# Kernel optimization log

Measured on AMD Instinct MI355X. Metric: run time of the kernel, lower is better.

Reference implementation:

```python
import jax, jax.numpy as jnp
import numpy as np

L, H, NH, KVH, HD, F, P, DLM, N = 4, 1024, 16, 2, 64, 4096, 4, 2048, 8192
QLEN = P + 1  # patch_size + 1 (special token prepended)
EPS = 1e-5


def _rms(x, w):
    return x * jax.lax.rsqrt(jnp.mean(x * x, axis=-1, keepdims=True) + EPS) * w


def _rotate_half(x):
    x1, x2 = jnp.split(x, 2, axis=-1)  # split_size = head_dim // 2
    return jnp.concatenate([-x2, x1], axis=-1)


def _rope_tables():
    pos = jnp.arange(QLEN, dtype=jnp.float32)
    inv_freq = 1.0 / (10000.0 ** (jnp.arange(0, HD, 2, dtype=jnp.float32) / HD))
    freqs = pos[:, None] * inv_freq[None, :]
    emb = jnp.concatenate([freqs, freqs], axis=-1)  # [QLEN, HD]
    scale = HD ** -0.25  # scale_factor baked into cos/sin as in source
    return jnp.cos(emb) * scale, jnp.sin(emb) * scale


def setup_inputs() -> dict:
    key = jax.random.key(0)
    ks = jax.random.split(key, 12)
    s = 0.02
    return {
        "audio_feat": jax.random.normal(ks[0], (N, P, 64), jnp.float32),
        "special_token": jax.random.normal(ks[1], (H,), jnp.float32) * s,
        "in_proj_w": jax.random.normal(ks[2], (64, H), jnp.float32) * s,
        "ln1_w": jnp.ones((L, H), jnp.float32),
        "wq": jax.random.normal(ks[3], (L, H, NH * HD), jnp.float32) * s,
        "wk": jax.random.normal(ks[4], (L, H, KVH * HD), jnp.float32) * s,
        "wv": jax.random.normal(ks[5], (L, H, KVH * HD), jnp.float32) * s,
        "wo": jax.random.normal(ks[6], (L, NH * HD, H), jnp.float32) * s,
        "ln2_w": jnp.ones((L, H), jnp.float32),
        "w_gate": jax.random.normal(ks[7], (L, H, F), jnp.float32) * s,
        "w_up": jax.random.normal(ks[8], (L, H, F), jnp.float32) * s,
        "w_down": jax.random.normal(ks[9], (L, F, H), jnp.float32) * s,
        "final_norm_w": jnp.ones((H,), jnp.float32),
        "enc_to_lm_w": jax.random.normal(ks[10], (H, DLM), jnp.float32) * s,
    }


def reference(audio_feat, special_token, in_proj_w, ln1_w, wq, wk, wv, wo,
              ln2_w, w_gate, w_up, w_down, final_norm_w, enc_to_lm_w):
    n = audio_feat.shape[0]
    h = audio_feat @ in_proj_w  # [N, P, H]
    sp = jnp.broadcast_to(special_token, (n, 1, H))
    h = jnp.concatenate([sp, h], axis=1)  # [N, QLEN, H]
    cos, sin = _rope_tables()
    g = NH // KVH  # num_key_value_groups
    for l in range(L):
        x = _rms(h, ln1_w[l])
        q = (x @ wq[l]).reshape(n, QLEN, NH, HD).transpose(0, 2, 1, 3)
        k = (x @ wk[l]).reshape(n, QLEN, KVH, HD).transpose(0, 2, 1, 3)
        v = (x @ wv[l]).reshape(n, QLEN, KVH, HD).transpose(0, 2, 1, 3)
        q = q * cos + _rotate_half(q) * sin
        k = k * cos + _rotate_half(k) * sin
        # explicit GQA repeat (cat-then-view == repeat along head axis)
        k = jnp.repeat(k, g, axis=1)
        v = jnp.repeat(v, g, axis=1)
        attn = jax.nn.softmax(jnp.einsum('bhqd,bhkd->bhqk', q, k), axis=-1)
        ao = jnp.einsum('bhqk,bhkd->bhqd', attn, v)
        ao = ao.transpose(0, 2, 1, 3).reshape(n, QLEN, NH * HD)
        h = h + ao @ wo[l]
        r = h
        x = _rms(h, ln2_w[l])
        h = r + (jax.nn.silu(x @ w_gate[l]) * (x @ w_up[l])) @ w_down[l]
    feat = _rms(h[:, 0], final_norm_w) @ enc_to_lm_w  # [N, DLM]
    return feat[None]  # [1, N, DLM]
```

## Files before the change

kernel.cpp:

```cpp
#include <hip/hip_runtime.h>
#include <hip/hip_bf16.h>

#define NSAMP 8192
#define QL 5
#define MTOK (NSAMP*QL)

typedef __hip_bfloat16 bf16;
typedef __attribute__((ext_vector_type(8))) __bf16 bf16x8;
typedef __attribute__((ext_vector_type(8))) unsigned short u16x8;
typedef __attribute__((ext_vector_type(4))) float f32x4;

__device__ __forceinline__ float bfu2f(unsigned short u){ return __uint_as_float(((unsigned)u)<<16); }
__device__ __forceinline__ float bf2f(bf16 v){ return __bfloat162float(v); }
__device__ __forceinline__ bf16  f2bf(float v){ return __float2bfloat16(v); }
__device__ __forceinline__ unsigned short f2bfu(float v){
  __hip_bfloat16 b = __float2bfloat16(v);
  return __builtin_bit_cast(unsigned short, b);
}

__device__ __forceinline__ void gload16(const void* g, void* l){
  __builtin_amdgcn_global_load_lds(
      (const __attribute__((address_space(1))) unsigned int*)g,
      (__attribute__((address_space(3))) unsigned int*)l, 16, 0, 0);
}

template<int RMAP>
__global__ __launch_bounds__(256) void k_transpose_cvt(const float* __restrict__ in,
                                                       bf16* __restrict__ out,
                                                       int K, int N){
  __shared__ float tile[32][33];
  int nb = blockIdx.x*32, kb = blockIdx.y*32;
  int tx = threadIdx.x, ty = threadIdx.y;
  #pragma unroll
  for (int j=0;j<4;j++)
    tile[ty+8*j][tx] = in[(size_t)(kb+ty+8*j)*N + nb+tx];
  __syncthreads();
  #pragma unroll
  for (int j=0;j<4;j++){
    int n = nb+ty+8*j;
    int R = (RMAP==0) ? n : (((n>>4)<<5) + (n&15) + (RMAP==2 ? 16 : 0));
    out[(size_t)R*K + kb+tx] = f2bf(tile[tx][ty+8*j]);
  }
}

__global__ __launch_bounds__(256) void k_cvt_bf16(const float* __restrict__ in,
                                                  bf16* __restrict__ out, int n4){
  int i = blockIdx.x*blockDim.x + threadIdx.x;
  if (i < n4){
    float4 v = ((const float4*)in)[i];
    out[4*i+0]=f2bf(v.x); out[4*i+1]=f2bf(v.y);
    out[4*i+2]=f2bf(v.z); out[4*i+3]=f2bf(v.w);
  }
}

__global__ __launch_bounds__(256) void k_fill_special(const float* __restrict__ sp,
                                                      bf16* __restrict__ h){
  int i = blockIdx.x*blockDim.x + threadIdx.x;
  int n = i >> 10, c = i & 1023;
  h[(size_t)n*QL*1024 + c] = f2bf(sp[c]);
}

__global__ void k_rope_tab(float* __restrict__ ctab, float* __restrict__ stab){
  int i = threadIdx.x;
  int t = i >> 6, d = i & 63, j = d & 31;
  float invf = __expf(-((float)j/32.0f) * logf(10000.0f));
  float ang  = (float)t * invf;
  const float s = 0.35355339059327373f;
  ctab[i] = cosf(ang)*s;
  stab[i] = sinf(ang)*s;
}

__global__ __launch_bounds__(256) void k_rmsnorm(const bf16* __restrict__ in,
                                                 const float* __restrict__ w,
                                                 bf16* __restrict__ out,
                                                 int nrows, int in_stride){
  int row  = blockIdx.x*4 + (threadIdx.x>>6);
  int lane = threadIdx.x & 63;
  if (row >= nrows) return;
  const bf16* p = in + (size_t)row*in_stride;
  float f[16]; float ss = 0.f;
  #pragma unroll
  for (int i=0;i<2;i++){
    u16x8 v = *(const u16x8*)(p + i*512 + lane*8);
    #pragma unroll
    for (int j=0;j<8;j++){ float x = bfu2f(v[j]); f[i*8+j] = x; ss += x*x; }
  }
  #pragma unroll
  for (int off=32; off; off>>=1) ss += __shfl_xor(ss, off);
  float inv = rsqrtf(ss * (1.0f/1024.0f) + 1e-5f);
  const float4* w4 = (const float4*)w;
  bf16* op = out + (size_t)row*1024;
  #pragma unroll
  for (int i=0;i<2;i++){
    int c = i*512 + lane*8;
    float4 wa = w4[c/4], wb = w4[c/4 + 1];
    u16x8 o;
    o[0]=f2bfu(f[i*8+0]*inv*wa.x); o[1]=f2bfu(f[i*8+1]*inv*wa.y);
    o[2]=f2bfu(f[i*8+2]*inv*wa.z); o[3]=f2bfu(f[i*8+3]*inv*wa.w);
    o[4]=f2bfu(f[i*8+4]*inv*wb.x); o[5]=f2bfu(f[i*8+5]*inv*wb.y);
    o[6]=f2bfu(f[i*8+6]*inv*wb.z); o[7]=f2bfu(f[i*8+7]*inv*wb.w);
    *(u16x8*)(op + c) = o;
  }
}

template<bool WRITEH>
__global__ __launch_bounds__(256) void k_addnorm(bf16* __restrict__ h,
                                                 const float* __restrict__ w,
                                                 const bf16* add,
                                                 bf16* out,
                                                 int nrows, int in_stride){
  int row  = blockIdx.x*4 + (threadIdx.x>>6);
  int lane = threadIdx.x & 63;
  if (row >= nrows) return;
  bf16* hp = h + (size_t)row*in_stride;
  const bf16* ap = add + (size_t)row*in_stride;
  float f[16]; float ss = 0.f;
  u16x8 hv[2], av[2];
  #pragma unroll
  for (int i=0;i<2;i++){
    hv[i] = *(const u16x8*)(hp + i*512 + lane*8);
    av[i] = *(const u16x8*)(ap + i*512 + lane*8);
  }
  #pragma unroll
  for (int i=0;i<2;i++)
    #pragma unroll
    for (int j=0;j<8;j++){
      float x = bfu2f(hv[i][j]) + bfu2f(av[i][j]);
      f[i*8+j] = x; ss += x*x;
    }
  if constexpr (WRITEH){
    #pragma unroll
    for (int i=0;i<2;i++){
      u16x8 o;
      #pragma unroll
      for (int j=0;j<8;j++) o[j] = f2bfu(f[i*8+j]);
      *(u16x8*)(hp + i*512 + lane*8) = o;
    }
  }
  #pragma unroll
  for (int off=32; off; off>>=1) ss += __shfl_xor(ss, off);
  float inv = rsqrtf(ss * (1.0f/1024.0f) + 1e-5f);
  const float4* w4 = (const float4*)w;
  bf16* op = out + (size_t)row*1024;
  #pragma unroll
  for (int i=0;i<2;i++){
    int c = i*512 + lane*8;
    float4 wa = w4[c/4], wb = w4[c/4 + 1];
    u16x8 o;
    o[0]=f2bfu(f[i*8+0]*inv*wa.x); o[1]=f2bfu(f[i*8+1]*inv*wa.y);
    o[2]=f2bfu(f[i*8+2]*inv*wa.z); o[3]=f2bfu(f[i*8+3]*inv*wa.w);
    o[4]=f2bfu(f[i*8+4]*inv*wb.x); o[5]=f2bfu(f[i*8+5]*inv*wb.y);
    o[6]=f2bfu(f[i*8+6]*inv*wb.z); o[7]=f2bfu(f[i*8+7]*inv*wb.w);
    *(u16x8*)(op + c) = o;
  }
}

template<int OUTMODE>
__device__ __forceinline__ void gemm256_impl(const bf16* __restrict__ A,
                                             const bf16* __restrict__ B,
                                             float* __restrict__ Cf,
                                             bf16* __restrict__ Cb,
                                             int M, int N, int K, int ldc){
  __shared__ bf16 lds[65536];
  char* ldsb = (char*)lds;
  const int tid  = threadIdx.x;
  const int wid  = tid >> 6, lane = tid & 63;
  const int wr   = wid >> 2, wc  = wid & 3;
  const int fr   = lane & 15, fq = lane >> 4;
  const int swz = (fr & 7) << 4;
  const int cs0 = (fq*16) ^ swz;
  const int cs1 = (fq*16 + 64) ^ swz;
  const int srcR = lane >> 3;
  const int srcC = ((lane & 7) ^ srcR) * 8;

  const int bm0 = blockIdx.x*256, bn0 = blockIdx.y*256;
  const bf16* gA = A + (size_t)bm0*K;
  const bf16* gB = B + (size_t)bn0*K;
  const int nt = K >> 6;

  const int aOff = (wr ? 16384 : 0);
  const int bOff = 32768 + ((wc>>1) ? 16384 : 0) + (wc&1)*8192;
  const char* aB0 = ldsb + aOff + fr*128 + cs0;
  const char* aB1 = ldsb + aOff + fr*128 + cs1;
  const char* bB0 = ldsb + bOff + fr*128 + cs0;
  const char* bB1 = ldsb + bOff + fr*128 + cs1;

  f32x4 acc[8][4] = {};
  bf16x8 aF[8][2], bF[4][2];

#define STAGE(p, t, h) {                                                        \
    const bf16* G_ = ((h) < 2) ? gA : gB;                                       \
    const int rb_ = ((h)&1) ? 128 : 0;                                          \
    const int k0_ = (t) << 6;                                                   \
    _Pragma("unroll")                                                           \
    for (int j_=0;j_<2;j_++){                                                   \
      int blk_ = j_*8 + wid;                                                    \
      gload16(G_ + (size_t)(rb_ + blk_*8 + srcR)*K + k0_ + srcC,               \
              ldsb + (p)*65536 + (h)*16384 + blk_*1024);                        \
    }                                                                           \
  }
#define RD_A(p, m0_) {                                                          \
    _Pragma("unroll")                                                           \
    for (int m_=0;m_<4;m_++)                                                    \
      _Pragma("unroll")                                                         \
      for (int ks_=0;ks_<2;ks_++)                                               \
        aF[(m0_)+m_][ks_] = *(const bf16x8*)((ks_ ? aB1 : aB0) + (p)*65536 + ((m0_)+m_)*2048); \
  }
#define RD_B(p, n0_) {                                                          \
    _Pragma("unroll")                                                           \
    for (int n_=0;n_<2;n_++)                                                    \
      _Pragma("unroll")                                                         \
      for (int ks_=0;ks_<2;ks_++)                                               \
        bF[(n0_)+n_][ks_] = *(const bf16x8*)((ks_ ? bB1 : bB0) + (p)*65536 + ((n0_)+n_)*2048); \
  }
#define MM(qm_, qn_) {                                                          \
    _Pragma("unroll")                                                           \
    for (int m_=0;m_<4;m_++)                                                    \
      _Pragma("unroll")                                                         \
      for (int n_=0;n_<2;n_++)                                                  \
        _Pragma("unroll")                                                       \
        for (int ks_=0;ks_<2;ks_++)                                             \
          acc[(qm_)*4+m_][(qn_)*2+n_] = __builtin_amdgcn_mfma_f32_16x16x32_bf16( \
              aF[(qm_)*4+m_][ks_], bF[(qn_)*2+n_][ks_], acc[(qm_)*4+m_][(qn_)*2+n_], 0,0,0); \
  }
#define LGKM0  asm volatile("s_waitcnt lgkmcnt(0)" ::: "memory"); __builtin_amdgcn_sched_barrier(0)
#define BAR    __builtin_amdgcn_s_barrier()

  STAGE(0, 0, 0); STAGE(0, 0, 1); STAGE(0, 0, 2); STAGE(0, 0, 3);
  if (nt > 1){ STAGE(1, 1, 0); STAGE(1, 1, 1); STAGE(1, 1, 2); STAGE(1, 1, 3); }
  if (nt > 1) asm volatile("s_waitcnt vmcnt(8)" ::: "memory");
  else        asm volatile("s_waitcnt vmcnt(0)" ::: "memory");
  BAR;

  for (int t = 0; t < nt; t++){
    const int cur = t & 1;
    const bool pf = (t + 2) < nt;
    RD_A(cur, 0); RD_B(cur, 0);
    BAR; LGKM0;
    __builtin_amdgcn_s_setprio(1); MM(0,0); __builtin_amdgcn_s_setprio(0);
    BAR;
    RD_A(cur, 4);
    BAR; LGKM0;
    __builtin_amdgcn_s_setprio(1); MM(1,0); __builtin_amdgcn_s_setprio(0);
    BAR;
    RD_B(cur, 2);
    if (pf) STAGE(cur, t+2, 0);
    BAR; LGKM0;
    __builtin_amdgcn_s_setprio(1); MM(0,1); __builtin_amdgcn_s_setprio(0);
    BAR;
    if (pf){ STAGE(cur, t+2, 1); STAGE(cur, t+2, 2); STAGE(cur, t+2, 3); }
    BAR;
    __builtin_amdgcn_s_setprio(1); MM(1,1); __builtin_amdgcn_s_setprio(0);
    if (t + 1 < nt){
      if (pf) asm volatile("s_waitcnt vmcnt(8)" ::: "memory");
      else    asm volatile("s_waitcnt vmcnt(0)" ::: "memory");
    }
    BAR;
  }

  #pragma unroll
  for (int m=0;m<8;m++){
    if constexpr (OUTMODE == 2){
      #pragma unroll
      for (int n2=0;n2<2;n2++){
        #pragma unroll
        for (int i=0;i<4;i++){
          int row = bm0 + wr*128 + m*16 + fq*4 + i;
          int col = (bn0>>1) + wc*32 + n2*16 + fr;
          float g = acc[m][n2*2][i], u = acc[m][n2*2+1][i];
          Cb[(size_t)row*ldc + col] = f2bf((g / (1.0f + __expf(-g))) * u);
        }
      }
    } else {
      #pragma unroll
      for (int n=0;n<4;n++){
        #pragma unroll
        for (int i=0;i<4;i++){
          int row = bm0 + wr*128 + m*16 + fq*4 + i;
          int col = bn0 + wc*64 + n*16 + fr;
          size_t idx = (size_t)row*ldc + col;
          if constexpr (OUTMODE == 0)      Cf[idx] = acc[m][n][i];
          else if constexpr (OUTMODE == 1) Cb[idx] = f2bf(acc[m][n][i]);
          else                             Cb[idx] = f2bf(bf2f(Cb[idx]) + acc[m][n][i]);
        }
      }
    }
  }
#undef STAGE
#undef RD_A
#undef RD_B
#undef MM
#undef LGKM0
#undef BAR
}

__global__ __launch_bounds__(512) void k_gemm_qkv(const bf16* A, const bf16* B, bf16* Cb, int M, int N, int K, int ldc){
  gemm256_impl<1>(A, B, nullptr, Cb, M, N, K, ldc);
}
__global__ __launch_bounds__(512) void k_gemm_wo(const bf16* A, const bf16* B, bf16* Cb, int M, int N, int K, int ldc){
  gemm256_impl<1>(A, B, nullptr, Cb, M, N, K, ldc);
}
__global__ __launch_bounds__(512) void k_gemm_gu(const bf16* A, const bf16* B, bf16* Cb, int M, int N, int K, int ldc){
  gemm256_impl<2>(A, B, nullptr, Cb, M, N, K, ldc);
}
__global__ __launch_bounds__(512) void k_gemm_down(const bf16* A, const bf16* B, bf16* Cb, int M, int N, int K, int ldc){
  gemm256_impl<1>(A, B, nullptr, Cb, M, N, K, ldc);
}
__global__ __launch_bounds__(512) void k_gemm_out(const bf16* A, const bf16* B, float* Cf, int M, int N, int K, int ldc){
  gemm256_impl<0>(A, B, Cf, nullptr, M, N, K, ldc);
}
__global__ __launch_bounds__(512) void k_gemm_wo_acc(const bf16* A, const bf16* B, bf16* Cb, int M, int N, int K, int ldc){
  gemm256_impl<3>(A, B, nullptr, Cb, M, N, K, ldc);
}
__global__ __launch_bounds__(512) void k_gemm_down_acc(const bf16* A, const bf16* B, bf16* Cb, int M, int N, int K, int ldc){
  gemm256_impl<3>(A, B, nullptr, Cb, M, N, K, ldc);
}

__global__ __launch_bounds__(256) void k_gemm_embed(const bf16* __restrict__ A,
                                                    const bf16* __restrict__ B0,
                                                    bf16* __restrict__ Cb,
                                                    int M, int N, int K, int ldc){
  constexpr int BM = 128, BN = 128, BK = 32;
  constexpr int WN = BN/2, NR = WN/16, MR = 4;
  __shared__ bf16 lA[BM*BK];
  __shared__ bf16 lB[BN*BK];
  int wid = threadIdx.x >> 6, lane = threadIdx.x & 63;
  int wr = wid >> 1, wc = wid & 1;
  int bm0 = blockIdx.x * BM, bn0 = blockIdx.y * BN;
  int fr = lane & 15, fq = lane >> 4;
  int rowInCh = lane >> 2, colInCh = (lane & 3)*8;
  f32x4 acc[MR][NR] = {};
  const bf16* gA = A + (size_t)bm0*K;
  const bf16* gB = B0 + (size_t)bn0*K;
  for (int k0 = 0; k0 < K; k0 += BK){
    #pragma unroll
    for (int i = 0; i < BM/64; i++){
      int ch = wid + 4*i;
      gload16(gA + (size_t)(16*ch + rowInCh)*K + k0 + colInCh, lA + 16*ch*BK);
    }
    #pragma unroll
    for (int i = 0; i < BN/64; i++){
      int ch = wid + 4*i;
      gload16(gB + (size_t)(16*ch + rowInCh)*K + k0 + colInCh, lB + 16*ch*BK);
    }
    __syncthreads();
    bf16x8 af[MR];
    #pragma unroll
    for (int m=0;m<MR;m++)
      af[m] = *(const bf16x8*)(lA + (wr*64 + m*16 + fr)*BK + fq*8);
    #pragma unroll
    for (int n=0;n<NR;n++){
      bf16x8 bfr = *(const bf16x8*)(lB + (wc*WN + n*16 + fr)*BK + fq*8);
      #pragma unroll
      for (int m=0;m<MR;m++)
        acc[m][n] = __builtin_amdgcn_mfma_f32_16x16x32_bf16(af[m], bfr, acc[m][n], 0,0,0);
    }
    __syncthreads();
  }
  #pragma unroll
  for (int m=0;m<MR;m++)
    #pragma unroll
    for (int n=0;n<NR;n++)
      #pragma unroll
      for (int i=0;i<4;i++){
        int row = bm0 + wr*64 + m*16 + fq*4 + i;
        int col = bn0 + wc*WN + n*16 + fr;
        size_t orow = (size_t)(row + (row>>2) + 1);
        Cb[orow*(size_t)ldc + col] = f2bf(acc[m][n][i]);
      }
}

__global__ __launch_bounds__(256) void k_attn(const bf16* __restrict__ qkv,
                                              bf16* __restrict__ xn,
                                              const float* __restrict__ ctab,
                                              const float* __restrict__ stab){
  int gw   = blockIdx.x*4 + (threadIdx.x>>6);
  int lane = threadIdx.x & 63;
  int sample = gw >> 4, head = gw & 15, kvh = head >> 3;

  float qf[QL], kf[QL], vf[QL];
  #pragma unroll
  for (int t=0;t<QL;t++){
    size_t r = (size_t)(sample*QL + t)*1280;
    qf[t] = bf2f(qkv[r + head*64 + lane]);
    kf[t] = bf2f(qkv[r + 1024 + kvh*64 + lane]);
    vf[t] = bf2f(qkv[r + 1152 + kvh*64 + lane]);
  }
  #pragma unroll
  for (int t=0;t<QL;t++){
    float c = ctab[t*64+lane], s = stab[t*64+lane];
    float qo = __shfl_xor(qf[t], 32);
    float ko = __shfl_xor(kf[t], 32);
    float rq = (lane < 32) ? -qo : qo;
    float rk = (lane < 32) ? -ko : ko;
    qf[t] = qf[t]*c + rq*s;
    kf[t] = kf[t]*c + rk*s;
  }
  float p[QL][QL];
  #pragma unroll
  for (int i=0;i<QL;i++)
    #pragma unroll
    for (int j=0;j<QL;j++) p[i][j] = qf[i]*kf[j];
  #pragma unroll
  for (int off=32; off; off>>=1){
    #pragma unroll
    for (int i=0;i<QL;i++)
      #pragma unroll
      for (int j=0;j<QL;j++) p[i][j] += __shfl_xor(p[i][j], off);
  }
  #pragma unroll
  for (int i=0;i<QL;i++){
    float mx = p[i][0];
    #pragma unroll
    for (int j=1;j<QL;j++) mx = fmaxf(mx, p[i][j]);
    float sum = 0.f;
    #pragma unroll
    for (int j=0;j<QL;j++){ p[i][j] = __expf(p[i][j]-mx); sum += p[i][j]; }
    float rs = 1.0f/sum;
    float o = 0.f;
    #pragma unroll
    for (int j=0;j<QL;j++) o += p[i][j]*vf[j];
    xn[((size_t)(sample*QL+i))*1024 + head*64 + lane] = f2bf(o*rs);
  }
}

__global__ void k_diag(float* out, float v){ out[0] = v; }

extern "C" void kernel_launch(void* const* d_in, const int* in_sizes, int n_in,
                              void* d_out, int out_size, void* d_ws, size_t ws_size,
                              hipStream_t stream){
  const float* audio = (const float*)d_in[0];
  const float* sp    = (const float*)d_in[1];
  const float* inpw  = (const float*)d_in[2];
  const float* ln1   = (const float*)d_in[3];
  const float* wq    = (const float*)d_in[4];
  const float* wk    = (const float*)d_in[5];
  const float* wv    = (const float*)d_in[6];
  const float* wo    = (const float*)d_in[7];
  const float* ln2   = (const float*)d_in[8];
  const float* wg    = (const float*)d_in[9];
  const float* wu    = (const float*)d_in[10];
  const float* wd    = (const float*)d_in[11];
  const float* fnw   = (const float*)d_in[12];
  const float* enc   = (const float*)d_in[13];
  float* out = (float*)d_out;
  char* ws = (char*)d_ws;

  size_t o_h=0,o_wqkv=0,o_wo=0,o_wgu=0,o_wd=0,o_ct=0,o_st=0,o_xn=0,o_u=0;
  size_t CH=0, RM=0;
  const size_t tierCH[5] = {8192, 8192, 4096, 2048, 1024};
  const size_t tierRM[5] = {40960, 20480, 10240, 5120, 2560};
  for (int t=0;t<5;t++){
    size_t ch = tierCH[t], R = ch*QL, rm = tierRM[t];
    size_t off = 0;
    auto al = [&](size_t b){ size_t o=off; off=(off+b+255)&~(size_t)255; return o; };
    o_h   = al((size_t)MTOK*1024*2);
    o_wqkv= al((size_t)1280*1024*2);
    o_wo  = al((size_t)1024*1024*2);
    o_wgu = al((size_t)8192*1024*2);
    o_wd  = al((size_t)1024*4096*2);
    o_ct  = al(QL*64*4);
    o_st  = al(QL*64*4);
    o_xn  = al(R*1024*2);
    size_t qkvB = R*1280*2, actB = rm*4096*2;
    o_u   = al(qkvB > actB ? qkvB : actB);
    if (off <= ws_size){ CH = ch; RM = rm; break; }
  }
  if (CH == 0){ k_diag<<<1,1,0,stream>>>(out, (float)ws_size); return; }
  const size_t R = CH*QL;

  bf16*  h     = (bf16*)(ws + o_h);
  bf16*  wqkvT = (bf16*)(ws + o_wqkv);
  bf16*  woT   = (bf16*)(ws + o_wo);
  bf16*  wguT  = (bf16*)(ws + o_wgu);
  bf16*  wdT   = (bf16*)(ws + o_wd);
  float* ctab  = (float*)(ws + o_ct);
  float* stab  = (float*)(ws + o_st);
  bf16*  xn    = (bf16*)(ws + o_xn);
  bf16*  qkv   = (bf16*)(ws + o_u);
  bf16*  act   = (bf16*)(ws + o_u);
  bf16*  ao    = (bf16*)(ws + o_u);
  bf16*  xc    = (bf16*)(ws + o_u);
  bf16*  af16  = (bf16*)(ws + o_u);
  bf16*  inprojT = wqkvT;
  bf16*  encT    = wguT;

  dim3 tb(32,8);
  k_rope_tab<<<1, 320, 0, stream>>>(ctab, stab);
  k_transpose_cvt<0><<<dim3(32, 2), tb, 0, stream>>>(inpw, inprojT, 64, 1024);
  k_cvt_bf16<<<(32768*64/4)/256, 256, 0, stream>>>(audio, af16, 32768*64/4);
  k_fill_special<<<NSAMP*1024/256, 256, 0, stream>>>(sp, h);
  k_gemm_embed<<<dim3(32768/128, 1024/128), 256, 0, stream>>>(
      af16, inprojT, h, 32768, 1024, 64, 1024);

  for (int l=0;l<4;l++){
    k_transpose_cvt<0><<<dim3(32, 32), tb, 0, stream>>>(wq + (size_t)l*1024*1024, wqkvT, 1024, 1024);
    k_transpose_cvt<0><<<dim3(4, 32),  tb, 0, stream>>>(wk + (size_t)l*1024*128,  wqkvT + (size_t)1024*1024, 1024, 128);
    k_transpose_cvt<0><<<dim3(4, 32),  tb, 0, stream>>>(wv + (size_t)l*1024*128,  wqkvT + (size_t)1152*1024, 1024, 128);
    k_transpose_cvt<0><<<dim3(32, 32), tb, 0, stream>>>(wo + (size_t)l*1024*1024, woT, 1024, 1024);
    k_transpose_cvt<1><<<dim3(128,32), tb, 0, stream>>>(wg + (size_t)l*1024*4096, wguT, 1024, 4096);
    k_transpose_cvt<2><<<dim3(128,32), tb, 0, stream>>>(wu + (size_t)l*1024*4096, wguT, 1024, 4096);
    k_transpose_cvt<0><<<dim3(32,128), tb, 0, stream>>>(wd + (size_t)l*4096*1024, wdT, 4096, 1024);

    if (CH == NSAMP){
      if (l == 0)
        k_rmsnorm<<<R/4, 256, 0, stream>>>(h, ln1 + l*1024, xn, (int)R, 1024);
      else
        k_addnorm<true><<<R/4, 256, 0, stream>>>(h, ln1 + l*1024, xn, xn, (int)R, 1024);
      k_gemm_qkv<<<dim3(R/256, 5), 512, 0, stream>>>(xn, wqkvT, qkv, (int)R, 1280, 1024, 1280);
      k_attn<<<CH*16/4, 256, 0, stream>>>(qkv, xn, ctab, stab);
      k_gemm_wo<<<dim3(R/256, 4), 512, 0, stream>>>(xn, woT, ao, (int)R, 1024, 1024, 1024);
      k_addnorm<true><<<R/4, 256, 0, stream>>>(h, ln2 + l*1024, ao, xn, (int)R, 1024);
      k_gemm_gu<<<dim3(R/256, 32), 512, 0, stream>>>(xn, wguT, act, (int)R, 8192, 1024, 4096);
      k_gemm_down<<<dim3(R/256, 4), 512, 0, stream>>>(act, wdT, xn, (int)R, 1024, 4096, 1024);
    } else {
      for (size_t c0 = 0; c0 < NSAMP; c0 += CH){
        size_t r0 = c0*QL;
        k_rmsnorm<<<R/4, 256, 0, stream>>>(h + r0*1024, ln1 + l*1024, xn, (int)R, 1024);
        k_gemm_qkv<<<dim3(R/256, 5), 512, 0, stream>>>(xn, wqkvT, qkv, (int)R, 1280, 1024, 1280);
        k_attn<<<CH*16/4, 256, 0, stream>>>(qkv, xn, ctab, stab);
        k_gemm_wo_acc<<<dim3(R/256, 4), 512, 0, stream>>>(xn, woT, h + r0*1024, (int)R, 1024, 1024, 1024);
        k_rmsnorm<<<R/4, 256, 0, stream>>>(h + r0*1024, ln2 + l*1024, xn, (int)R, 1024);
        for (size_t m0 = 0; m0 < R; m0 += RM){
          k_gemm_gu<<<dim3(RM/256, 32), 512, 0, stream>>>(xn + m0*1024, wguT, act, (int)RM, 8192, 1024, 4096);
          k_gemm_down_acc<<<dim3(RM/256, 4), 512, 0, stream>>>(act, wdT, h + (r0+m0)*1024, (int)RM, 1024, 4096, 1024);
        }
      }
    }
  }

  k_transpose_cvt<0><<<dim3(64, 32), tb, 0, stream>>>(enc, encT, 1024, 2048);
  if (CH == NSAMP){
    k_addnorm<false><<<NSAMP/4, 256, 0, stream>>>(h, fnw, xn, xc, NSAMP, QL*1024);
    k_gemm_out<<<dim3(NSAMP/256, 2048/256), 512, 0, stream>>>(xc, encT, out, NSAMP, 2048, 1024, 2048);
  } else {
    for (size_t c0 = 0; c0 < NSAMP; c0 += CH){
      k_rmsnorm<<<CH/4, 256, 0, stream>>>(h + c0*QL*1024, fnw, xn, (int)CH, QL*1024);
      k_gemm_out<<<dim3(CH/256, 2048/256), 512, 0, stream>>>(xn, encT, out + c0*2048, (int)CH, 2048, 1024, 2048);
    }
  }
}
```

Baseline: 7.372 ms.

## Restructure GEMM LDS wait schedule, merge per-layer weight transposes, unify chunked flow

The GEMM main loop now issues all LDS fragment reads for a K-tile up front and uses partial lgkmcnt waits instead of a full wait before each MFMA quarter. It also removes several barriers, so LDS reads overlap with matrix math. The seven per-layer weight transpose launches are merged into one kernel with block-index dispatch. Host orchestration is restructured to keep a full-size xn buffer with chunked QKV/attn, Wo/addnorm and MLP loops, dropping the accumulate-output GEMM variants. Removing barriers risks LDS hazards if the waits are miscounted.

```diff
diff --git a/kernel.cpp b/kernel.cpp
--- a/kernel.cpp
+++ b/kernel.cpp
@@ -24,23 +24,46 @@
       (__attribute__((address_space(3))) unsigned int*)l, 16, 0, 0);
 }
 
-template<int RMAP>
+__device__ __forceinline__ void transpose_body(const float* __restrict__ in,
+                                               bf16* __restrict__ out,
+                                               int K, int N, int nb, int kb, int rmap){
+  __shared__ float tile[32][33];
+  int tx = threadIdx.x, ty = threadIdx.y;
+  #pragma unroll
+  for (int j=0;j<4;j++)
+    tile[ty+8*j][tx] = in[(size_t)(kb+ty+8*j)*N + nb+tx];
+  __syncthreads();
+  #pragma unroll
+  for (int j=0;j<4;j++){
+    int n = nb+ty+8*j;
+    int R = (rmap==0) ? n : (((n>>4)<<5) + (n&15) + (rmap==2 ? 16 : 0));
+    out[(size_t)R*K + kb+tx] = f2bf(tile[tx][ty+8*j]);
+  }
+}
+
 __global__ __launch_bounds__(256) void k_transpose_cvt(const float* __restrict__ in,
                                                        bf16* __restrict__ out,
                                                        int K, int N){
-  __shared__ float tile[32][33];
-  int nb = blockIdx.x*32, kb = blockIdx.y*32;
-  int tx = threadIdx.x, ty = threadIdx.y;
-  #pragma unroll
-  for (int j=0;j<4;j++)
-    tile[ty+8*j][tx] = in[(size_t)(kb+ty+8*j)*N + nb+tx];
-  __syncthreads();
-  #pragma unroll
-  for (int j=0;j<4;j++){
-    int n = nb+ty+8*j;
-    int R = (RMAP==0) ? n : (((n>>4)<<5) + (n&15) + (RMAP==2 ? 16 : 0));
-    out[(size_t)R*K + kb+tx] = f2bf(tile[tx][ty+8*j]);
-  }
+  transpose_body(in, out, K, N, blockIdx.x*32, blockIdx.y*32, 0);
+}
+
+__global__ __launch_bounds__(256) void k_transpose_layer(
+    const float* __restrict__ wq, const float* __restrict__ wk,
+    const float* __restrict__ wv, const float* __restrict__ wo,
+    const float* __restrict__ wg, const float* __restrict__ wu,
+    const float* __restrict__ wd,
+    bf16* __restrict__ wqkvT, bf16* __restrict__ woT,
+    bf16* __restrict__ wguT, bf16* __restrict__ wdT){
+  int id = blockIdx.x;
+  const float* in; bf16* out; int K=1024, N=1024, nbx=32, rmap=0;
+  if (id < 1024){ in=wq; out=wqkvT; }
+  else if (id < 1152){ id-=1024; in=wk; out=wqkvT+(size_t)1024*1024; N=128; nbx=4; }
+  else if (id < 1280){ id-=1152; in=wv; out=wqkvT+(size_t)1152*1024; N=128; nbx=4; }
+  else if (id < 2304){ id-=1280; in=wo; out=woT; }
+  else if (id < 6400){ id-=2304; in=wg; out=wguT; N=4096; nbx=128; rmap=1; }
+  else if (id < 10496){ id-=6400; in=wu; out=wguT; N=4096; nbx=128; rmap=2; }
+  else { id-=10496; in=wd; out=wdT; K=4096; N=1024; nbx=32; }
+  transpose_body(in, out, K, N, (id % nbx)*32, (id / nbx)*32, rmap);
 }
 
 __global__ __launch_bounds__(256) void k_cvt_bf16(const float* __restrict__ in,
@@ -223,7 +246,7 @@
           acc[(qm_)*4+m_][(qn_)*2+n_] = __builtin_amdgcn_mfma_f32_16x16x32_bf16( \
               aF[(qm_)*4+m_][ks_], bF[(qn_)*2+n_][ks_], acc[(qm_)*4+m_][(qn_)*2+n_], 0,0,0); \
   }
-#define LGKM0  asm volatile("s_waitcnt lgkmcnt(0)" ::: "memory"); __builtin_amdgcn_sched_barrier(0)
+#define SBAR   __builtin_amdgcn_sched_barrier(0)
 #define BAR    __builtin_amdgcn_s_barrier()
 
   STAGE(0, 0, 0); STAGE(0, 0, 1); STAGE(0, 0, 2); STAGE(0, 0, 3);
@@ -236,20 +259,19 @@
     const int cur = t & 1;
     const bool pf = (t + 2) < nt;
     RD_A(cur, 0); RD_B(cur, 0);
-    BAR; LGKM0;
+    SBAR;
+    RD_A(cur, 4); RD_B(cur, 2);
+    BAR;
+    SBAR; asm volatile("s_waitcnt lgkmcnt(12)" ::: "memory"); SBAR;
     __builtin_amdgcn_s_setprio(1); MM(0,0); __builtin_amdgcn_s_setprio(0);
     BAR;
-    RD_A(cur, 4);
-    BAR; LGKM0;
+    SBAR; asm volatile("s_waitcnt lgkmcnt(0)" ::: "memory"); SBAR;
     __builtin_amdgcn_s_setprio(1); MM(1,0); __builtin_amdgcn_s_setprio(0);
     BAR;
-    RD_B(cur, 2);
     if (pf) STAGE(cur, t+2, 0);
-    BAR; LGKM0;
     __builtin_amdgcn_s_setprio(1); MM(0,1); __builtin_amdgcn_s_setprio(0);
     BAR;
     if (pf){ STAGE(cur, t+2, 1); STAGE(cur, t+2, 2); STAGE(cur, t+2, 3); }
-    BAR;
     __builtin_amdgcn_s_setprio(1); MM(1,1); __builtin_amdgcn_s_setprio(0);
     if (t + 1 < nt){
       if (pf) asm volatile("s_waitcnt vmcnt(8)" ::: "memory");
@@ -279,9 +301,8 @@
           int row = bm0 + wr*128 + m*16 + fq*4 + i;
           int col = bn0 + wc*64 + n*16 + fr;
           size_t idx = (size_t)row*ldc + col;
-          if constexpr (OUTMODE == 0)      Cf[idx] = acc[m][n][i];
-          else if constexpr (OUTMODE == 1) Cb[idx] = f2bf(acc[m][n][i]);
-          else                             Cb[idx] = f2bf(bf2f(Cb[idx]) + acc[m][n][i]);
+          if constexpr (OUTMODE == 0) Cf[idx] = acc[m][n][i];
+          else                        Cb[idx] = f2bf(acc[m][n][i]);
         }
       }
     }
@@ -290,7 +311,7 @@
 #undef RD_A
 #undef RD_B
 #undef MM
-#undef LGKM0
+#undef SBAR
 #undef BAR
 }
 
@@ -308,12 +329,6 @@
 }
 __global__ __launch_bounds__(512) void k_gemm_out(const bf16* A, const bf16* B, float* Cf, int M, int N, int K, int ldc){
   gemm256_impl<0>(A, B, Cf, nullptr, M, N, K, ldc);
-}
-__global__ __launch_bounds__(512) void k_gemm_wo_acc(const bf16* A, const bf16* B, bf16* Cb, int M, int N, int K, int ldc){
-  gemm256_impl<3>(A, B, nullptr, Cb, M, N, K, ldc);
-}
-__global__ __launch_bounds__(512) void k_gemm_down_acc(const bf16* A, const bf16* B, bf16* Cb, int M, int N, int K, int ldc){
-  gemm256_impl<3>(A, B, nullptr, Cb, M, N, K, ldc);
 }
 
 __global__ __launch_bounds__(256) void k_gemm_embed(const bf16* __restrict__ A,
@@ -448,10 +463,10 @@
 
   size_t o_h=0,o_wqkv=0,o_wo=0,o_wgu=0,o_wd=0,o_ct=0,o_st=0,o_xn=0,o_u=0;
   size_t CH=0, RM=0;
-  const size_t tierCH[5] = {8192, 8192, 4096, 2048, 1024};
-  const size_t tierRM[5] = {40960, 20480, 10240, 5120, 2560};
-  for (int t=0;t<5;t++){
-    size_t ch = tierCH[t], R = ch*QL, rm = tierRM[t];
+  const size_t tierCH[6] = {8192, 8192, 8192, 4096, 2048, 1024};
+  const size_t tierRM[6] = {40960, 20480, 10240, 10240, 5120, 2560};
+  for (int t=0;t<6;t++){
+    size_t ch = tierCH[t], rm = tierRM[t];
     size_t off = 0;
     auto al = [&](size_t b){ size_t o=off; off=(off+b+255)&~(size_t)255; return o; };
     o_h   = al((size_t)MTOK*1024*2);
@@ -461,13 +476,14 @@
     o_wd  = al((size_t)1024*4096*2);
     o_ct  = al(QL*64*4);
     o_st  = al(QL*64*4);
-    o_xn  = al(R*1024*2);
-    size_t qkvB = R*1280*2, actB = rm*4096*2;
-    o_u   = al(qkvB > actB ? qkvB : actB);
+    o_xn  = al((size_t)MTOK*1024*2);
+    size_t qkvB = ch*QL*1280*2, aoB = ch*QL*1024*2;
+    size_t actB = rm*4096*2,    xcB = (size_t)NSAMP*1024*2;
+    size_t ub = qkvB; if (aoB>ub) ub=aoB; if (actB>ub) ub=actB; if (xcB>ub) ub=xcB;
+    o_u   = al(ub);
     if (off <= ws_size){ CH = ch; RM = rm; break; }
   }
   if (CH == 0){ k_diag<<<1,1,0,stream>>>(out, (float)ws_size); return; }
-  const size_t R = CH*QL;
 
   bf16*  h     = (bf16*)(ws + o_h);
   bf16*  wqkvT = (bf16*)(ws + o_wqkv);
@@ -477,66 +493,52 @@
   float* ctab  = (float*)(ws + o_ct);
   float* stab  = (float*)(ws + o_st);
   bf16*  xn    = (bf16*)(ws + o_xn);
-  bf16*  qkv   = (bf16*)(ws + o_u);
-  bf16*  act   = (bf16*)(ws + o_u);
-  bf16*  ao    = (bf16*)(ws + o_u);
-  bf16*  xc    = (bf16*)(ws + o_u);
-  bf16*  af16  = (bf16*)(ws + o_u);
+  bf16*  ubuf  = (bf16*)(ws + o_u);
   bf16*  inprojT = wqkvT;
   bf16*  encT    = wguT;
 
   dim3 tb(32,8);
   k_rope_tab<<<1, 320, 0, stream>>>(ctab, stab);
-  k_transpose_cvt<0><<<dim3(32, 2), tb, 0, stream>>>(inpw, inprojT, 64, 1024);
-  k_cvt_bf16<<<(32768*64/4)/256, 256, 0, stream>>>(audio, af16, 32768*64/4);
+  k_transpose_cvt<<<dim3(32, 2), tb, 0, stream>>>(inpw, inprojT, 64, 1024);
+  k_cvt_bf16<<<(32768*64/4)/256, 256, 0, stream>>>(audio, ubuf, 32768*64/4);
   k_fill_special<<<NSAMP*1024/256, 256, 0, stream>>>(sp, h);
   k_gemm_embed<<<dim3(32768/128, 1024/128), 256, 0, stream>>>(
-      af16, inprojT, h, 32768, 1024, 64, 1024);
+      ubuf, inprojT, h, 32768, 1024, 64, 1024);
 
   for (int l=0;l<4;l++){
-    k_transpose_cvt<0><<<dim3(32, 32), tb, 0, stream>>>(wq + (size_t)l*1024*1024, wqkvT, 1024, 1024);
-    k_transpose_cvt<0><<<dim3(4, 32),  tb, 0, stream>>>(wk + (size_t)l*1024*128,  wqkvT + (size_t)1024*1024, 1024, 128);
-    k_transpose_cvt<0><<<dim3(4, 32),  tb, 0, stream>>>(wv + (size_t)l*1024*128,  wqkvT + (size_t)1152*1024, 1024, 128);
-    k_transpose_cvt<0><<<dim3(32, 32), tb, 0, stream>>>(wo + (size_t)l*1024*1024, woT, 1024, 1024);
-    k_transpose_cvt<1><<<dim3(128,32), tb, 0, stream>>>(wg + (size_t)l*1024*4096, wguT, 1024, 4096);
-    k_transpose_cvt<2><<<dim3(128,32), tb, 0, stream>>>(wu + (size_t)l*1024*4096, wguT, 1024, 4096);
-    k_transpose_cvt<0><<<dim3(32,128), tb, 0, stream>>>(wd + (size_t)l*4096*1024, wdT, 4096, 1024);
-
-    if (CH == NSAMP){
-      if (l == 0)
-        k_rmsnorm<<<R/4, 256, 0, stream>>>(h, ln1 + l*1024, xn, (int)R, 1024);
-      else
-        k_addnorm<true><<<R/4, 256, 0, stream>>>(h, ln1 + l*1024, xn, xn, (int)R, 1024);
-      k_gemm_qkv<<<dim3(R/256, 5), 512, 0, stream>>>(xn, wqkvT, qkv, (int)R, 1280, 1024, 1280);
-      k_attn<<<CH*16/4, 256, 0, stream>>>(qkv, xn, ctab, stab);
-      k_gemm_wo<<<dim3(R/256, 4), 512, 0, stream>>>(xn, woT, ao, (int)R, 1024, 1024, 1024);
-      k_addnorm<true><<<R/4, 256, 0, stream>>>(h, ln2 + l*1024, ao, xn, (int)R, 1024);
-      k_gemm_gu<<<dim3(R/256, 32), 512, 0, stream>>>(xn, wguT, act, (int)R, 8192, 1024, 4096);
-      k_gemm_down<<<dim3(R/256, 4), 512, 0, stream>>>(act, wdT, xn, (int)R, 1024, 4096, 1024);
-    } else {
-      for (size_t c0 = 0; c0 < NSAMP; c0 += CH){
-        size_t r0 = c0*QL;
-        k_rmsnorm<<<R/4, 256, 0, stream>>>(h + r0*1024, ln1 + l*1024, xn, (int)R, 1024);
-        k_gemm_qkv<<<dim3(R/256, 5), 512, 0, stream>>>(xn, wqkvT, qkv, (int)R, 1280, 1024, 1280);
-        k_attn<<<CH*16/4, 256, 0, stream>>>(qkv, xn, ctab, stab);
-        k_gemm_wo_acc<<<dim3(R/256, 4), 512, 0, stream>>>(xn, woT, h + r0*1024, (int)R, 1024, 1024, 1024);
-        k_rmsnorm<<<R/4, 256, 0, stream>>>(h + r0*1024, ln2 + l*1024, xn, (int)R, 1024);
-        for (size_t m0 = 0; m0 < R; m0 += RM){
-          k_gemm_gu<<<dim3(RM/256, 32), 512, 0, stream>>>(xn + m0*1024, wguT, act, (int)RM, 8192, 1024, 4096);
-          k_gemm_down_acc<<<dim3(RM/256, 4), 512, 0, stream>>>(act, wdT, h + (r0+m0)*1024, (int)RM, 1024, 4096, 1024);
-        }
-      }
-    }
-  }
-
-  k_transpose_cvt<0><<<dim3(64, 32), tb, 0, stream>>>(enc, encT, 1024, 2048);
-  if (CH == NSAMP){
-    k_addnorm<false><<<NSAMP/4, 256, 0, stream>>>(h, fnw, xn, xc, NSAMP, QL*1024);
-    k_gemm_out<<<dim3(NSAMP/256, 2048/256), 512, 0, stream>>>(xc, encT, out, NSAMP, 2048, 1024, 2048);
-  } else {
+    k_transpose_layer<<<14592, tb, 0, stream>>>(
+        wq + (size_t)l*1024*1024, wk + (size_t)l*1024*128, wv + (size_t)l*1024*128,
+        wo + (size_t)l*1024*1024, wg + (size_t)l*1024*4096, wu + (size_t)l*1024*4096,
+        wd + (size_t)l*4096*1024, wqkvT, woT, wguT, wdT);
+
+    if (l == 0)
+      k_rmsnorm<<<MTOK/4, 256, 0, stream>>>(h, ln1, xn, MTOK, 1024);
+    else
+      k_addnorm<true><<<MTOK/4, 256, 0, stream>>>(h, ln1 + l*1024, xn, xn, MTOK, 1024);
+
     for (size_t c0 = 0; c0 < NSAMP; c0 += CH){
-      k_rmsnorm<<<CH/4, 256, 0, stream>>>(h + c0*QL*1024, fnw, xn, (int)CH, QL*1024);
-      k_gemm_out<<<dim3(CH/256, 2048/256), 512, 0, stream>>>(xn, encT, out + c0*2048, (int)CH, 2048, 1024, 2048);
-    }
-  }
-}
+      size_t r0 = c0*QL, Rc = CH*QL;
+      k_gemm_qkv<<<dim3(Rc/256, 5), 512, 0, stream>>>(
+          xn + r0*1024, wqkvT, ubuf, (int)Rc, 1280, 1024, 1280);
+      k_attn<<<CH*16/4, 256, 0, stream>>>(ubuf, xn + r0*1024, ctab, stab);
+    }
+    for (size_t c0 = 0; c0 < NSAMP; c0 += CH){
+      size_t r0 = c0*QL, Rc = CH*QL;
+      k_gemm_wo<<<dim3(Rc/256, 4), 512, 0, stream>>>(
+          xn + r0*1024, woT, ubuf, (int)Rc, 1024, 1024, 1024);
+      k_addnorm<true><<<Rc/4, 256, 0, stream>>>(
+          h + r0*1024, ln2 + l*1024, ubuf, xn + r0*1024, (int)Rc, 1024);
+    }
+    for (size_t m0 = 0; m0 < MTOK; m0 += RM){
+      k_gemm_gu<<<dim3(RM/256, 32), 512, 0, stream>>>(
+          xn + m0*1024, wguT, ubuf, (int)RM, 8192, 1024, 4096);
+      k_gemm_down<<<dim3(RM/256, 4), 512, 0, stream>>>(
+          ubuf, wdT, xn + m0*1024, (int)RM, 1024, 4096, 1024);
+    }
+  }
+
+  k_transpose_cvt<<<dim3(64, 32), tb, 0, stream>>>(enc, encT, 1024, 2048);
+  k_addnorm<false><<<NSAMP/4, 256, 0, stream>>>(h, fnw, xn, ubuf, NSAMP, QL*1024);
+  k_gemm_out<<<dim3(NSAMP/256, 2048/256), 512, 0, stream>>>(
+      ubuf, encT, out, NSAMP, 2048, 1024, 2048);
+}
```

New measurement: 8.878 ms. 20.4% more time.
